# Kernel optimization log

Measured on AMD Instinct MI355X. Metric: run time of the kernel, lower is better.

## Reference

```python
import jax, jax.numpy as jnp
import numpy as np

NB_POOLS = 256


def setup_inputs() -> dict:
    key = jax.random.key(0)
    x = jax.random.normal(key, (32, 32, 32, 512), dtype=jnp.float32)
    return {"x": x}


def reference(x) -> jnp.ndarray:
    B, R, C, F = x.shape
    nb_maps = R * C
    x3 = x.reshape(B, nb_maps, F)
    # self-correlation: (B, nb_maps, nb_maps), normalized by feature count
    corr = jnp.einsum('bmf,bnf->bmn', x3, x3) / F
    corr = corr.reshape(B, R, C, nb_maps)
    # percentile ranks into the descending-sorted correlation values
    ranks = jnp.round(jnp.linspace(1.0, nb_maps - 1, NB_POOLS)).astype(jnp.int32)
    # full descending sort along last axis (matches tf.nn.top_k k=nb_maps)
    x_sort = -jnp.sort(-corr, axis=-1)
    x_pool = x_sort[..., ranks]  # (B, R, C, NB_POOLS)
    return x_pool
```

## Files before the change

### kernel.cpp

```cpp
#include <hip/hip_runtime.h>


#define NMAPS 1024
#define FDIM 512
#define TM 16
#define NT 256

typedef __attribute__((ext_vector_type(8))) short short8_t;
typedef __attribute__((ext_vector_type(4))) float f32x4;
typedef _Float16 h2 __attribute__((ext_vector_type(2)));

#define SELD 0x03020504u
#define SELA 0x07060100u

__device__ __forceinline__ h2 h2min(h2 a, h2 b) { return __builtin_elementwise_min(a, b); }
__device__ __forceinline__ h2 h2max(h2 a, h2 b) { return __builtin_elementwise_max(a, b); }

__device__ __forceinline__ unsigned h2u(h2 x) { union { h2 h; unsigned u; } t; t.h = x; return t.u; }
__device__ __forceinline__ h2 u2h(unsigned x) { union { h2 h; unsigned u; } t; t.u = x; return t.h; }

__device__ __forceinline__ h2 h2swap(h2 v) {
  unsigned u = h2u(v);
  return u2h((u >> 16) | (u << 16));
}

__device__ __forceinline__ h2 h2shfl_xor(h2 v, int m) {
  union { h2 h; int i; } u;
  u.h = v;
  u.i = __shfl_xor(u.i, m, 64);
  return u.h;
}

__device__ __forceinline__ void ce_pair(h2& a, h2& b, bool d) {
  h2 mn = h2min(a, b), mx = h2max(a, b);
  a = d ? mx : mn;
  b = d ? mn : mx;
}

__device__ __forceinline__ h2 ce1(h2 w, unsigned sel) {
  h2 s = h2swap(w);
  h2 mn = h2min(w, s), mx = h2max(w, s);
#if __has_builtin(__builtin_amdgcn_perm)
  return u2h(__builtin_amdgcn_perm(h2u(mx), h2u(mn), sel));
#else
  h2 rd; rd[0] = mx[0]; rd[1] = mn[1];
  h2 ra; ra[0] = mn[0]; ra[1] = mx[1];
  return (sel == SELD) ? rd : ra;
#endif
}

__device__ __forceinline__ void intra_merge16(h2 w[8], bool d, unsigned sel) {
  ce_pair(w[0], w[4], d); ce_pair(w[1], w[5], d); ce_pair(w[2], w[6], d); ce_pair(w[3], w[7], d);
  ce_pair(w[0], w[2], d); ce_pair(w[1], w[3], d); ce_pair(w[4], w[6], d); ce_pair(w[5], w[7], d);
  ce_pair(w[0], w[1], d); ce_pair(w[2], w[3], d); ce_pair(w[4], w[5], d); ce_pair(w[6], w[7], d);
#pragma unroll
  for (int u = 0; u < 8; ++u) w[u] = ce1(w[u], sel);
}

__device__ __forceinline__ void sort16(h2 w[8], bool d, unsigned sd, unsigned si) {
  w[0] = ce1(w[0], sd); w[1] = ce1(w[1], si); w[2] = ce1(w[2], sd); w[3] = ce1(w[3], si);
  w[4] = ce1(w[4], sd); w[5] = ce1(w[5], si); w[6] = ce1(w[6], sd); w[7] = ce1(w[7], si);
  ce_pair(w[0], w[1], d); ce_pair(w[2], w[3], !d); ce_pair(w[4], w[5], d); ce_pair(w[6], w[7], !d);
  w[0] = ce1(w[0], sd); w[1] = ce1(w[1], sd); w[2] = ce1(w[2], si); w[3] = ce1(w[3], si);
  w[4] = ce1(w[4], sd); w[5] = ce1(w[5], sd); w[6] = ce1(w[6], si); w[7] = ce1(w[7], si);
  ce_pair(w[0], w[2], d); ce_pair(w[1], w[3], d); ce_pair(w[4], w[6], !d); ce_pair(w[5], w[7], !d);
  ce_pair(w[0], w[1], d); ce_pair(w[2], w[3], d); ce_pair(w[4], w[5], !d); ce_pair(w[6], w[7], !d);
  w[0] = ce1(w[0], sd); w[1] = ce1(w[1], sd); w[2] = ce1(w[2], sd); w[3] = ce1(w[3], sd);
  w[4] = ce1(w[4], si); w[5] = ce1(w[5], si); w[6] = ce1(w[6], si); w[7] = ce1(w[7], si);
  intra_merge16(w, d, sd);
}

__device__ __forceinline__ void cross_ce(h2 w[8], int m, bool keepmax) {
#pragma unroll
  for (int u = 0; u < 8; ++u) {
    h2 p = h2shfl_xor(w[u], m);
    h2 mn = h2min(w[u], p), mx = h2max(w[u], p);
    w[u] = keepmax ? mx : mn;
  }
}

template<int K>
__device__ __forceinline__ void bitonic_stage(h2 w8[8], int lane) {
  const bool laneDesc = (K >= 16) ? ((lane & (K >> 4)) == 0) : true;
#pragma unroll
  for (int j = 512; j >= 16; j >>= 1) {
    if (j > (K >> 1)) continue;
    const int m = j >> 4;
    const bool keepmax = (((lane & m) == 0) == laneDesc);
#pragma unroll
    for (int u = 0; u < 8; ++u) {
      h2 p = h2shfl_xor(w8[u], m);
      h2 mn = h2min(w8[u], p), mx = h2max(w8[u], p);
      w8[u] = keepmax ? mx : mn;
    }
  }
#pragma unroll
  for (int j = 8; j >= 2; j >>= 1) {
    if (j > (K >> 1)) continue;
    const int jw = j >> 1;
#pragma unroll
    for (int u = 0; u < 8; ++u) {
      if ((u & jw) == 0) {
        const int v = u | jw;
        const bool desc = (K <= 8) ? (((2 * u) & K) == 0) : laneDesc;
        h2 mn = h2min(w8[u], w8[v]), mx = h2max(w8[u], w8[v]);
        w8[u] = desc ? mx : mn;
        w8[v] = desc ? mn : mx;
      }
    }
  }
#pragma unroll
  for (int u = 0; u < 8; ++u) {
    const bool desc = (K <= 8) ? (((2 * u) & K) == 0) : laneDesc;
    h2 s = h2swap(w8[u]);
    h2 mn = h2min(w8[u], s), mx = h2max(w8[u], s);
    h2 rd = (h2){mx[0], mn[1]};
    h2 ra = (h2){mn[0], mx[1]};
    w8[u] = desc ? rd : ra;
  }
}

template<int K>
__device__ __forceinline__ void bitonic_stage_tail(h2 w8[8], int lane) {
  const bool laneDesc = ((lane & (K >> 4)) == 0);
#pragma unroll
  for (int j = 512; j >= 16; j >>= 1) {
    if (j > (K >> 1)) continue;
    const int m = j >> 4;
    cross_ce(w8, m, ((lane & m) == 0) == laneDesc);
  }
  intra_merge16(w8, laneDesc, laneDesc ? SELD : SELA);
}

__device__ __forceinline__ void run_bitonic(h2 w8[8], int lane) {
  bitonic_stage<2>(w8, lane);
  bitonic_stage<4>(w8, lane);
  bitonic_stage<8>(w8, lane);
  bitonic_stage<16>(w8, lane);
  bitonic_stage<32>(w8, lane);
  bitonic_stage<64>(w8, lane);
  bitonic_stage<128>(w8, lane);
  bitonic_stage<256>(w8, lane);
  bitonic_stage<512>(w8, lane);
  bitonic_stage<1024>(w8, lane);
}

__global__ __launch_bounds__(256) void cvt_bf16_kernel(const float* __restrict__ x,
                                                       short* __restrict__ xw, int n8) {
  int i = blockIdx.x * 256 + threadIdx.x;
  if (i >= n8) return;
  const float4* x4 = reinterpret_cast<const float4*>(x);
  float4 a = x4[i * 2], c = x4[i * 2 + 1];
  float f[8] = {a.x, a.y, a.z, a.w, c.x, c.y, c.z, c.w};
  union { short8_t v; short s[8]; } o;
#pragma unroll
  for (int j = 0; j < 8; ++j) {
    unsigned u = __float_as_uint(f[j]);
    u += 0x7fffu + ((u >> 16) & 1u);
    o.s[j] = (short)(u >> 16);
  }
  reinterpret_cast<short8_t*>(xw)[i] = o.v;
}

__global__ __launch_bounds__(NT) void corr_gemm_tiled(const short* __restrict__ xw,
                                                      unsigned* __restrict__ corrW) {
  __shared__ short Asm[128 * 32];
  __shared__ short Bsm[128 * 32];
  const int tid = threadIdx.x;
  const int b = blockIdx.y;
  const int it = blockIdx.x >> 3, jt = blockIdx.x & 7;
  const int i0 = it * 128, j0 = jt * 128;
  const int lane = tid & 63;
  const int wid = tid >> 6;
  const int lr = lane & 15;
  const int kg = lane >> 4;
  const int wr = wid >> 1, wc = wid & 1;
  const short* Xb = xw + (size_t)b * NMAPS * FDIM;

  f32x4 acc[4][4];
#pragma unroll
  for (int fm = 0; fm < 4; ++fm)
#pragma unroll
    for (int fn = 0; fn < 4; ++fn) acc[fm][fn] = (f32x4){0.f, 0.f, 0.f, 0.f};

  for (int kt = 0; kt < 16; ++kt) {
    __syncthreads();
#pragma unroll
    for (int rp = 0; rp < 2; ++rp) {
      const int idx = rp * 256 + tid;
      const int r = idx >> 2, s = idx & 3;
      const short* gA = Xb + (size_t)(i0 + r) * FDIM + kt * 32 + s * 8;
      const short* gB = Xb + (size_t)(j0 + r) * FDIM + kt * 32 + s * 8;
      __builtin_amdgcn_global_load_lds(
          (const __attribute__((address_space(1))) unsigned*)gA,
          (__attribute__((address_space(3))) unsigned*)(Asm + idx * 8), 16, 0, 0);
      __builtin_amdgcn_global_load_lds(
          (const __attribute__((address_space(1))) unsigned*)gB,
          (__attribute__((address_space(3))) unsigned*)(Bsm + idx * 8), 16, 0, 0);
    }
    __syncthreads();

    short8_t a[4], bf[4];
#pragma unroll
    for (int fm = 0; fm < 4; ++fm)
      a[fm] = *reinterpret_cast<const short8_t*>(Asm + (wr * 64 + fm * 16 + lr) * 32 + kg * 8);
#pragma unroll
    for (int fn = 0; fn < 4; ++fn)
      bf[fn] = *reinterpret_cast<const short8_t*>(Bsm + (wc * 64 + fn * 16 + lr) * 32 + kg * 8);
#pragma unroll
    for (int fm = 0; fm < 4; ++fm)
#pragma unroll
      for (int fn = 0; fn < 4; ++fn)
        acc[fm][fn] = __builtin_amdgcn_mfma_f32_16x16x32_bf16(bf[fn], a[fm], acc[fm][fn], 0, 0, 0);
  }

  const bool D0 = (wc == 0);
  const bool d16 = ((kg & 1) == 0) ? D0 : !D0;
  const unsigned sd16 = d16 ? SELD : SELA, si16 = d16 ? SELA : SELD;
  const bool d32 = ((kg & 2) == 0) ? D0 : !D0;
  const float sc = 1.f / FDIM;

#pragma unroll
  for (int fm = 0; fm < 4; ++fm) {
    h2 w[8];
#pragma unroll
    for (int fn = 0; fn < 4; ++fn) {
      w[2 * fn] = (h2){(_Float16)(acc[fm][fn][0] * sc), (_Float16)(acc[fm][fn][1] * sc)};
      w[2 * fn + 1] = (h2){(_Float16)(acc[fm][fn][2] * sc), (_Float16)(acc[fm][fn][3] * sc)};
    }
    sort16(w, d16, sd16, si16);
    cross_ce(w, 16, ((kg & 1) == 0) == d32);
    intra_merge16(w, d32, d32 ? SELD : SELA);
    cross_ce(w, 32, ((kg & 2) == 0) == D0);
    cross_ce(w, 16, ((kg & 1) == 0) == D0);
    intra_merge16(w, D0, D0 ? SELD : SELA);
    const size_t roww = ((size_t)b * NMAPS + i0 + wr * 64 + fm * 16 + lr) * 512;
    const int wq = (j0 >> 1) + wc * 32 + kg * 8;
    union { h2 h[4]; uint4 u; } s0, s1;
    s0.h[0] = w[0]; s0.h[1] = w[1]; s0.h[2] = w[2]; s0.h[3] = w[3];
    s1.h[0] = w[4]; s1.h[1] = w[5]; s1.h[2] = w[6]; s1.h[3] = w[7];
    *reinterpret_cast<uint4*>(corrW + roww + wq) = s0.u;
    *reinterpret_cast<uint4*>(corrW + roww + wq + 4) = s1.u;
  }
}

__global__ __launch_bounds__(256) void sort_rows_kernel(const unsigned* __restrict__ corrW,
                                                        float* __restrict__ out) {
  const int tid = threadIdx.x;
  const int lane = tid & 63;
  const int row = blockIdx.x * 4 + (tid >> 6);
  const uint4* r4 = reinterpret_cast<const uint4*>(corrW + (size_t)row * 512);

  h2 w8[8];
  {
    union { uint4 u; h2 h[4]; } a, c;
    a.u = r4[lane * 2];
    c.u = r4[lane * 2 + 1];
    w8[0] = a.h[0]; w8[1] = a.h[1]; w8[2] = a.h[2]; w8[3] = a.h[3];
    w8[4] = c.h[0]; w8[5] = c.h[1]; w8[6] = c.h[2]; w8[7] = c.h[3];
  }

  bitonic_stage_tail<128>(w8, lane);
  bitonic_stage_tail<256>(w8, lane);
  bitonic_stage_tail<512>(w8, lane);
  bitonic_stage_tail<1024>(w8, lane);

  float* orow = out + (size_t)row * 256;
#pragma unroll
  for (int u = 0; u < 8; ++u) {
#pragma unroll
    for (int hh = 0; hh < 2; ++hh) {
      const int i = lane * 16 + 2 * u + hh;
      const int p = (int)rint((double)(i - 1) * (255.0 / 1022.0));
      const int rk = (int)rint(1.0 + (double)p * (1022.0 / 255.0));
      if (rk == i) orow[p] = (float)w8[u][hh];
    }
  }
}

__global__ __launch_bounds__(NT) void selfcorr_mfma_kernel(const short* __restrict__ xw,
                                                           float* __restrict__ out) {
  __shared__ alignas(16) h2 SH[TM * 512];
  const int tid = threadIdx.x;
  const int b = blockIdx.y;
  const int m0 = blockIdx.x * TM;
  const int lane = tid & 63;
  const int wid = tid >> 6;
  const int lr = lane & 15;
  const int kg = lane >> 4;
  const int wc = wid * 256;
  const short* Xb = xw + (size_t)b * NMAPS * FDIM;

  f32x4 acc[16];
#pragma unroll
  for (int t = 0; t < 16; ++t) acc[t] = (f32x4){0.f, 0.f, 0.f, 0.f};

  for (int kk = 0; kk < 16; ++kk) {
    const short8_t* base = reinterpret_cast<const short8_t*>(Xb + kk * 32 + kg * 8);
    short8_t afrag = base[(size_t)(m0 + lr) * 64];
    short8_t bfrag[16];
#pragma unroll
    for (int t = 0; t < 16; ++t) bfrag[t] = base[(size_t)(wc + t * 16 + lr) * 64];
#pragma unroll
    for (int t = 0; t < 16; ++t)
      acc[t] = __builtin_amdgcn_mfma_f32_16x16x32_bf16(bfrag[t], afrag, acc[t], 0, 0, 0);
  }

  {
    const int xorv = (lr & 7) << 2;
#pragma unroll
    for (int t = 0; t < 16; ++t) {
      h2 lo = (h2){(_Float16)(acc[t][0] * (1.f / FDIM)), (_Float16)(acc[t][1] * (1.f / FDIM))};
      h2 hi = (h2){(_Float16)(acc[t][2] * (1.f / FDIM)), (_Float16)(acc[t][3] * (1.f / FDIM))};
      const int W = (wc >> 1) + t * 8 + kg * 2;
      const int phys = lr * 512 + (W ^ xorv);
      union { h2 h[2]; uint2 u; } pk;
      pk.h[0] = lo; pk.h[1] = hi;
      *reinterpret_cast<uint2*>(&SH[phys]) = pk.u;
    }
  }
  __syncthreads();

  const int rowbase = wid * 4;
  for (int rr = rowbase; rr < rowbase + 4; ++rr) {
    const int rx = (rr & 7) << 2;
    h2 w8[8];
#pragma unroll
    for (int q = 0; q < 2; ++q) {
      const int p4 = rr * 512 + ((lane * 8 + q * 4) ^ rx);
      union { uint4 u; h2 h[4]; } un;
      un.u = *reinterpret_cast<const uint4*>(&SH[p4]);
      w8[q * 4 + 0] = un.h[0]; w8[q * 4 + 1] = un.h[1];
      w8[q * 4 + 2] = un.h[2]; w8[q * 4 + 3] = un.h[3];
    }
    run_bitonic(w8, lane);
#pragma unroll
    for (int q = 0; q < 2; ++q) {
      const int p4 = rr * 512 + ((lane * 8 + q * 4) ^ rx);
      union { uint4 u; h2 h[4]; } un;
      un.h[0] = w8[q * 4 + 0]; un.h[1] = w8[q * 4 + 1];
      un.h[2] = w8[q * 4 + 2]; un.h[3] = w8[q * 4 + 3];
      *reinterpret_cast<uint4*>(&SH[p4]) = un.u;
    }
  }
  __builtin_amdgcn_wave_barrier();

#pragma unroll
  for (int i = 0; i < 16; ++i) {
    const int rr = rowbase + (i >> 2);
    const int p = lane + ((i & 3) << 6);
    const int rank = (int)rint(1.0 + (double)p * (1022.0 / 255.0));
    const int Wr = (rank >> 1) ^ ((rr & 7) << 2);
    h2 hv = SH[rr * 512 + Wr];
    out[((size_t)(b * NMAPS + m0 + rr) << 8) + p] = (float)hv[rank & 1];
  }
}

__device__ __forceinline__ int sw4(int row, int c4) {
  return (row << 8) | (c4 ^ ((c4 >> 3) & 7));
}
__device__ __forceinline__ void ce(float& a, float& b, bool desc) {
  float mn = fminf(a, b);
  float mx = fmaxf(a, b);
  a = desc ? mx : mn;
  b = desc ? mn : mx;
}

__global__ __launch_bounds__(NT) void selfcorr_pool_kernel(const float* __restrict__ x,
                                                           float* __restrict__ out) {
  __shared__ float lds[TM * NMAPS];
  float4* S4 = reinterpret_cast<float4*>(lds);
  const int tid = threadIdx.x;
  const int b = blockIdx.y;
  const int m0 = blockIdx.x * TM;
  const float4* Xb = reinterpret_cast<const float4*>(x) + (size_t)b * NMAPS * (FDIM / 4);

  float4* A4 = reinterpret_cast<float4*>(lds);
#pragma unroll
  for (int idx = tid; idx < TM * (FDIM / 4); idx += NT) {
    A4[idx] = Xb[(m0 + (idx >> 7)) * 128 + (idx & 127)];
  }
  __syncthreads();

  float acc[TM][4];
#pragma unroll
  for (int m = 0; m < TM; ++m)
#pragma unroll
    for (int j = 0; j < 4; ++j) acc[m][j] = 0.0f;

  float4 nb0 = Xb[(tid + 0) * 128];
  float4 nb1 = Xb[(tid + 256) * 128];
  float4 nb2 = Xb[(tid + 512) * 128];
  float4 nb3 = Xb[(tid + 768) * 128];
  for (int k4 = 0; k4 < 128; ++k4) {
    float4 b0 = nb0, b1 = nb1, b2 = nb2, b3 = nb3;
    const int kn = (k4 < 127) ? (k4 + 1) : 127;
    nb0 = Xb[(tid + 0) * 128 + kn];
    nb1 = Xb[(tid + 256) * 128 + kn];
    nb2 = Xb[(tid + 512) * 128 + kn];
    nb3 = Xb[(tid + 768) * 128 + kn];
#pragma unroll
    for (int m = 0; m < TM; ++m) {
      float4 a = A4[m * 128 + k4];
      acc[m][0] += a.x * b0.x + a.y * b0.y + a.z * b0.z + a.w * b0.w;
      acc[m][1] += a.x * b1.x + a.y * b1.y + a.z * b1.z + a.w * b1.w;
      acc[m][2] += a.x * b2.x + a.y * b2.y + a.z * b2.z + a.w * b2.w;
      acc[m][3] += a.x * b3.x + a.y * b3.y + a.z * b3.z + a.w * b3.w;
    }
  }
  __syncthreads();

#pragma unroll
  for (int m = 0; m < TM; ++m) {
#pragma unroll
    for (int j = 0; j < 4; ++j) {
      const int n = tid + (j << 8);
      lds[sw4(m, n >> 2) * 4 + (n & 3)] = acc[m][j] * (1.0f / FDIM);
    }
  }
  __syncthreads();

#pragma unroll
  for (int c = 0; c < 2; ++c) {
    const int cid = tid + (c << 8);
    const int row = cid >> 5;
    const int chunk = cid & 31;
    float r[32];
#pragma unroll
    for (int q = 0; q < 8; ++q) {
      float4 t = S4[sw4(row, (chunk << 3) + q)];
      r[q * 4 + 0] = t.x; r[q * 4 + 1] = t.y; r[q * 4 + 2] = t.z; r[q * 4 + 3] = t.w;
    }
    const bool D = ((chunk & 1) == 0);
#pragma unroll
    for (int k2 = 2; k2 <= 32; k2 <<= 1) {
#pragma unroll
      for (int j = k2 >> 1; j > 0; j >>= 1) {
#pragma unroll
        for (int i = 0; i < 32; ++i) {
          if ((i & j) == 0) ce(r[i], r[i | j], ((i & k2) == 0) ? D : !D);
        }
      }
    }
#pragma unroll
    for (int q = 0; q < 8; ++q) {
      S4[sw4(row, (chunk << 3) + q)] =
          make_float4(r[q * 4 + 0], r[q * 4 + 1], r[q * 4 + 2], r[q * 4 + 3]);
    }
  }
  __syncthreads();

  for (int k = 64; k <= NMAPS; k <<= 1) {
    for (int j = k >> 1; j >= 32; j >>= 1) {
      const int j4 = j >> 2;
      const int kq = k >> 2;
#pragma unroll
      for (int q = 0; q < 8; ++q) {
        const int g = tid + (q << 8);
        const int row = g >> 7;
        const int v = g & 127;
        const int i4 = ((v & ~(j4 - 1)) << 1) | (v & (j4 - 1));
        const bool desc = ((i4 & kq) == 0);
        const int ia = sw4(row, i4);
        const int ib = sw4(row, i4 + j4);
        float4 va = S4[ia];
        float4 vb = S4[ib];
        float4 lo, hi;
        lo.x = fminf(va.x, vb.x); hi.x = fmaxf(va.x, vb.x);
        lo.y = fminf(va.y, vb.y); hi.y = fmaxf(va.y, vb.y);
        lo.z = fminf(va.z, vb.z); hi.z = fmaxf(va.z, vb.z);
        lo.w = fminf(va.w, vb.w); hi.w = fmaxf(va.w, vb.w);
        S4[ia] = desc ? hi : lo;
        S4[ib] = desc ? lo : hi;
      }
      __syncthreads();
    }
#pragma unroll
    for (int c = 0; c < 2; ++c) {
      const int cid = tid + (c << 8);
      const int row = cid >> 5;
      const int chunk = cid & 31;
      const bool D = (((chunk << 5) & k) == 0);
      float r[32];
#pragma unroll
      for (int q = 0; q < 8; ++q) {
        float4 t = S4[sw4(row, (chunk << 3) + q)];
        r[q * 4 + 0] = t.x; r[q * 4 + 1] = t.y; r[q * 4 + 2] = t.z; r[q * 4 + 3] = t.w;
      }
#pragma unroll
      for (int j = 16; j > 0; j >>= 1) {
#pragma unroll
        for (int i = 0; i < 32; ++i) {
          if ((i & j) == 0) ce(r[i], r[i | j], D);
        }
      }
#pragma unroll
      for (int q = 0; q < 8; ++q) {
        S4[sw4(row, (chunk << 3) + q)] =
            make_float4(r[q * 4 + 0], r[q * 4 + 1], r[q * 4 + 2], r[q * 4 + 3]);
      }
    }
    __syncthreads();
  }

  const int p = tid;
  const int rank = (int)rint(1.0 + (double)p * (1022.0 / 255.0));
#pragma unroll
  for (int m = 0; m < TM; ++m) {
    out[((size_t)(b * NMAPS + m0 + m) << 8) + p] = lds[sw4(m, rank >> 2) * 4 + (rank & 3)];
  }
}

extern "C" void kernel_launch(void* const* d_in, const int* in_sizes, int n_in,
                              void* d_out, int out_size, void* d_ws, size_t ws_size,
                              hipStream_t stream) {
  const float* x = reinterpret_cast<const float*>(d_in[0]);
  float* out = reinterpret_cast<float*>(d_out);
  const int nelem = in_sizes[0];
  const int B = nelem / (NMAPS * FDIM);
  const size_t need_split = (size_t)nelem * 2 + (size_t)B * NMAPS * NMAPS * 2;
  if (ws_size >= need_split) {
    short* xw = reinterpret_cast<short*>(d_ws);
    unsigned* corrW = reinterpret_cast<unsigned*>((char*)d_ws + (size_t)nelem * 2);
    const int n8 = nelem / 8;
    hipLaunchKernelGGL(cvt_bf16_kernel, dim3((n8 + 255) / 256), dim3(256), 0, stream, x, xw, n8);
    hipLaunchKernelGGL(corr_gemm_tiled, dim3(64, B), dim3(NT), 0, stream, xw, corrW);
    hipLaunchKernelGGL(sort_rows_kernel, dim3(B * NMAPS / 4), dim3(256), 0, stream, corrW, out);
  } else if (ws_size >= (size_t)nelem * 2) {
    short* xw = reinterpret_cast<short*>(d_ws);
    const int n8 = nelem / 8;
    hipLaunchKernelGGL(cvt_bf16_kernel, dim3((n8 + 255) / 256), dim3(256), 0, stream, x, xw, n8);
    hipLaunchKernelGGL(selfcorr_mfma_kernel, dim3(NMAPS / TM, B), dim3(NT), 0, stream, xw, out);
  } else {
    hipLaunchKernelGGL(selfcorr_pool_kernel, dim3(NMAPS / TM, B), dim3(NT), 0, stream, x, out);
  }
}
```

Measured before the change: 169.9 us.

## Double-buffer LDS tiles with XOR swizzle and defer correlation scaling to output

```diff
diff --git a/kernel.cpp b/kernel.cpp
--- a/kernel.cpp
+++ b/kernel.cpp
@@ -164,8 +164,8 @@
 
 __global__ __launch_bounds__(NT) void corr_gemm_tiled(const short* __restrict__ xw,
                                                       unsigned* __restrict__ corrW) {
-  __shared__ short Asm[128 * 32];
-  __shared__ short Bsm[128 * 32];
+  __shared__ short Asm[2][128 * 32];
+  __shared__ short Bsm[2][128 * 32];
   const int tid = threadIdx.x;
   const int b = blockIdx.y;
   const int it = blockIdx.x >> 3, jt = blockIdx.x & 7;
@@ -177,56 +177,82 @@
   const int wr = wid >> 1, wc = wid & 1;
   const short* Xb = xw + (size_t)b * NMAPS * FDIM;
 
+  const int idxs[2] = {tid, tid + 256};
+  int srcOff[2];
+#pragma unroll
+  for (int rp = 0; rp < 2; ++rp) {
+    const int r = idxs[rp] >> 2;
+    const int s = (idxs[rp] & 3) ^ ((r >> 1) & 3);
+    srcOff[rp] = r * FDIM + s * 8;
+  }
+
   f32x4 acc[4][4];
 #pragma unroll
   for (int fm = 0; fm < 4; ++fm)
 #pragma unroll
     for (int fn = 0; fn < 4; ++fn) acc[fm][fn] = (f32x4){0.f, 0.f, 0.f, 0.f};
 
+#define STAGE(buf, kt)                                                                 \
+  {                                                                                    \
+    _Pragma("unroll") for (int rp = 0; rp < 2; ++rp) {                                 \
+      const short* gA = Xb + (size_t)i0 * FDIM + srcOff[rp] + (kt) * 32;               \
+      const short* gB = Xb + (size_t)j0 * FDIM + srcOff[rp] + (kt) * 32;               \
+      __builtin_amdgcn_global_load_lds(                                                \
+          (const __attribute__((address_space(1))) unsigned*)gA,                       \
+          (__attribute__((address_space(3))) unsigned*)(Asm[buf] + idxs[rp] * 8), 16,  \
+          0, 0);                                                                       \
+      __builtin_amdgcn_global_load_lds(                                                \
+          (const __attribute__((address_space(1))) unsigned*)gB,                       \
+          (__attribute__((address_space(3))) unsigned*)(Bsm[buf] + idxs[rp] * 8), 16,  \
+          0, 0);                                                                       \
+    }                                                                                  \
+  }
+
+  int aOff[4], bOff[4];
+#pragma unroll
+  for (int f = 0; f < 4; ++f) {
+    const int ra = wr * 64 + f * 16 + lr;
+    const int rb = wc * 64 + f * 16 + lr;
+    aOff[f] = ra * 32 + (kg ^ ((ra >> 1) & 3)) * 8;
+    bOff[f] = rb * 32 + (kg ^ ((rb >> 1) & 3)) * 8;
+  }
+
+  STAGE(0, 0);
+  __syncthreads();
+
   for (int kt = 0; kt < 16; ++kt) {
-    __syncthreads();
-#pragma unroll
-    for (int rp = 0; rp < 2; ++rp) {
-      const int idx = rp * 256 + tid;
-      const int r = idx >> 2, s = idx & 3;
-      const short* gA = Xb + (size_t)(i0 + r) * FDIM + kt * 32 + s * 8;
-      const short* gB = Xb + (size_t)(j0 + r) * FDIM + kt * 32 + s * 8;
-      __builtin_amdgcn_global_load_lds(
-          (const __attribute__((address_space(1))) unsigned*)gA,
-          (__attribute__((address_space(3))) unsigned*)(Asm + idx * 8), 16, 0, 0);
-      __builtin_amdgcn_global_load_lds(
-          (const __attribute__((address_space(1))) unsigned*)gB,
-          (__attribute__((address_space(3))) unsigned*)(Bsm + idx * 8), 16, 0, 0);
-    }
-    __syncthreads();
+    const int cur = kt & 1;
+    if (kt < 15) STAGE(cur ^ 1, kt + 1);
 
     short8_t a[4], bf[4];
 #pragma unroll
     for (int fm = 0; fm < 4; ++fm)
-      a[fm] = *reinterpret_cast<const short8_t*>(Asm + (wr * 64 + fm * 16 + lr) * 32 + kg * 8);
+      a[fm] = *reinterpret_cast<const short8_t*>(Asm[cur] + aOff[fm]);
 #pragma unroll
     for (int fn = 0; fn < 4; ++fn)
-      bf[fn] = *reinterpret_cast<const short8_t*>(Bsm + (wc * 64 + fn * 16 + lr) * 32 + kg * 8);
+      bf[fn] = *reinterpret_cast<const short8_t*>(Bsm[cur] + bOff[fn]);
 #pragma unroll
     for (int fm = 0; fm < 4; ++fm)
 #pragma unroll
       for (int fn = 0; fn < 4; ++fn)
         acc[fm][fn] = __builtin_amdgcn_mfma_f32_16x16x32_bf16(bf[fn], a[fm], acc[fm][fn], 0, 0, 0);
-  }
+
+    __syncthreads();
+  }
+#undef STAGE
 
   const bool D0 = (wc == 0);
   const bool d16 = ((kg & 1) == 0) ? D0 : !D0;
   const unsigned sd16 = d16 ? SELD : SELA, si16 = d16 ? SELA : SELD;
   const bool d32 = ((kg & 2) == 0) ? D0 : !D0;
-  const float sc = 1.f / FDIM;
 
 #pragma unroll
   for (int fm = 0; fm < 4; ++fm) {
     h2 w[8];
 #pragma unroll
     for (int fn = 0; fn < 4; ++fn) {
-      w[2 * fn] = (h2){(_Float16)(acc[fm][fn][0] * sc), (_Float16)(acc[fm][fn][1] * sc)};
-      w[2 * fn + 1] = (h2){(_Float16)(acc[fm][fn][2] * sc), (_Float16)(acc[fm][fn][3] * sc)};
+      w[2 * fn] = (h2){(_Float16)acc[fm][fn][0], (_Float16)acc[fm][fn][1]};
+      w[2 * fn + 1] = (h2){(_Float16)acc[fm][fn][2], (_Float16)acc[fm][fn][3]};
     }
     sort16(w, d16, sd16, si16);
     cross_ce(w, 16, ((kg & 1) == 0) == d32);
@@ -273,7 +299,7 @@
       const int i = lane * 16 + 2 * u + hh;
       const int p = (int)rint((double)(i - 1) * (255.0 / 1022.0));
       const int rk = (int)rint(1.0 + (double)p * (1022.0 / 255.0));
-      if (rk == i) orow[p] = (float)w8[u][hh];
+      if (rk == i) orow[p] = (float)w8[u][hh] * (1.f / FDIM);
     }
   }
 }
```

Measured after the change: 167.8 us. Within noise of the previous version (-1.2%).
